# Kernel optimization log

Measured on AMD Instinct MI355X. Metric: run time of the kernel, lower is better.

The kernel has to match this reference:

```python
import jax, jax.numpy as jnp
import numpy as np
from jax import lax

BN_EPS = 1e-5
ARC_EPS = 1e-7
M = 0.5   # margin
S = 64.0  # scale


def _conv_block(x, w, g, b, a, stride):
    # Conv2d(bias=False, VALID) + BatchNorm2d (training mode, batch stats) + PReLU
    y = lax.conv_general_dilated(x, w, (stride, stride), 'VALID',
                                 dimension_numbers=('NCHW', 'OIHW', 'NCHW'))
    mu = y.mean((0, 2, 3), keepdims=True)
    var = ((y - mu) ** 2).mean((0, 2, 3), keepdims=True)
    y = (y - mu) * lax.rsqrt(var + BN_EPS) * g.reshape(1, -1, 1, 1) + b.reshape(1, -1, 1, 1)
    return jnp.where(y > 0, y, a * y)


def setup_inputs() -> dict:
    key = jax.random.key(0)
    ks = jax.random.split(key, 16)
    N = 4096
    d = {}
    d['x'] = jax.random.normal(ks[0], (N, 1, 28, 28), jnp.float32)
    d['labels'] = jax.random.randint(ks[1], (N,), 0, 10)
    conv_shapes = [(32, 1, 1, 1), (64, 32, 3, 3), (32, 64, 1, 1),
                   (64, 32, 3, 3), (32, 64, 1, 1), (64, 32, 3, 3)]
    for i, s in enumerate(conv_shapes):
        fan_in = s[1] * s[2] * s[3]
        d[f'cw{i}'] = jax.random.normal(ks[2 + i], s, jnp.float32) / np.sqrt(fan_in)
        d[f'bg{i}'] = jnp.ones((s[0],), jnp.float32)
        d[f'bb{i}'] = jnp.zeros((s[0],), jnp.float32)
        d[f'pa{i}'] = jnp.full((), 0.25, jnp.float32)  # nn.PReLU() single param
    d['lw1'] = jax.random.normal(ks[8], (128, 1024), jnp.float32) * (1.0 / np.sqrt(1024))
    d['lg1'] = jnp.ones((128,), jnp.float32)
    d['lb1'] = jnp.zeros((128,), jnp.float32)
    d['pl1'] = jnp.full((), 0.25, jnp.float32)
    d['lw2'] = jax.random.normal(ks[9], (2, 128), jnp.float32) * (1.0 / np.sqrt(128))
    d['lb2'] = jnp.zeros((2,), jnp.float32)
    d['aw'] = jax.random.normal(ks[10], (10, 2), jnp.float32) * 0.2  # ArcLoss fc weight (out, in)
    return d


def reference(x, labels, cw0, cw1, cw2, cw3, cw4, cw5,
              bg0, bb0, bg1, bb1, bg2, bb2, bg3, bb3, bg4, bb4, bg5, bb5,
              pa0, pa1, pa2, pa3, pa4, pa5,
              lw1, lg1, lb1, pl1, lw2, lb2, aw):
    strides = (1, 2, 1, 2, 1, 1)
    ws = (cw0, cw1, cw2, cw3, cw4, cw5)
    gs = (bg0, bg1, bg2, bg3, bg4, bg5)
    bs = (bb0, bb1, bb2, bb3, bb4, bb5)
    pas = (pa0, pa1, pa2, pa3, pa4, pa5)
    h = x
    for w, g, b, a, st in zip(ws, gs, bs, pas, strides):
        h = _conv_block(h, w, g, b, a, st)  # final: (N, 64, 4, 4)
    flat = h.reshape(h.shape[0], -1)        # (N, 1024)
    z = flat @ lw1.T                         # (N, 128)
    mu = z.mean(0)
    var = ((z - mu) ** 2).mean(0)
    z = (z - mu) * lax.rsqrt(var + BN_EPS) * lg1 + lb1
    z = jnp.where(z > 0, z, pl1 * z)
    features = z @ lw2.T + lb2               # (N, 2)

    # ArcLoss. NOTE: original torch code's weight-normalization loop is a no-op
    # (rebinds local var), so fc weight is used UN-normalized; only x is normalized.
    xn = features / jnp.linalg.norm(features, axis=-1, keepdims=True)
    wf = xn @ aw.T                           # (N, 10) logits
    n = wf.shape[0]
    tgt = wf[jnp.arange(n), labels]          # vectorized diag gather
    num = S * jnp.cos(jnp.arccos(jnp.clip(tgt, -1.0 + ARC_EPS, 1.0 - ARC_EPS)) + M)
    # vectorized exclusion sum: sum_j exp(s*wf[i,j]) minus the target column
    den = jnp.exp(num) + jnp.sum(jnp.exp(S * wf), axis=1) - jnp.exp(S * tgt)
    loss = -jnp.mean(num - jnp.log(den))
    return (features, wf, loss)
```

## Files before the change

### kernel.cpp

```cpp
#include <hip/hip_runtime.h>
#include <hip/hip_bf16.h>
#include <hip/hip_fp16.h>
#include <math.h>


typedef __attribute__((ext_vector_type(8))) short s16x8;
typedef __attribute__((ext_vector_type(8))) _Float16 f16x8;
typedef __attribute__((ext_vector_type(2))) _Float16 h16x2;
typedef __attribute__((ext_vector_type(16))) float f32x16;

__device__ __forceinline__ unsigned short f2bf(float f) {
  __hip_bfloat16 h = __float2bfloat16(f);
  unsigned short u;
  __builtin_memcpy(&u, &h, 2);
  return u;
}
__device__ __forceinline__ float bf2f(unsigned short h) {
  union { unsigned int u; float f; } t; t.u = ((unsigned int)h) << 16; return t.f;
}
__device__ __forceinline__ unsigned short f2h(float f) {
  _Float16 h = (_Float16)f;
  unsigned short u;
  __builtin_memcpy(&u, &h, 2);
  return u;
}

__device__ void dRedX(const float* __restrict__ x, float* __restrict__ part, int b) {
  int tid = threadIdx.x;
  const float4* x4 = (const float4*)x;
  float s = 0.f, q = 0.f;
  for (size_t i = (size_t)b * 256 + tid; i < 802816; i += (size_t)512 * 256) {
    float4 v = x4[i];
    s += v.x + v.y + v.z + v.w;
    q += v.x * v.x + v.y * v.y + v.z * v.z + v.w * v.w;
  }
#pragma unroll
  for (int off = 32; off; off >>= 1) {
    s += __shfl_down(s, off);
    q += __shfl_down(q, off);
  }
  __shared__ float ls[4][2];
  int w = tid >> 6;
  if ((tid & 63) == 0) { ls[w][0] = s; ls[w][1] = q; }
  __syncthreads();
  if (tid == 0) {
    part[b * 2]     = ls[0][0] + ls[1][0] + ls[2][0] + ls[3][0];
    part[b * 2 + 1] = ls[0][1] + ls[1][1] + ls[2][1] + ls[3][1];
  }
}

__device__ void dPrepW(const float* __restrict__ cw1, unsigned short* __restrict__ wf) {
  int tid = threadIdx.x;
  int lane = tid & 63, fb = tid >> 6;
  int m = lane & 31, kg = lane >> 5;
  for (int pass = 0; pass < 9; pass++) {
    int f = pass * 4 + fb;
    int tap = f >> 2, rem = f & 3, kt = rem >> 1, nt = rem & 1;
    int o = nt * 32 + m;
    int kb = kt * 16 + kg * 8;
    union { s16x8 v; unsigned short e[8]; } u;
#pragma unroll
    for (int j = 0; j < 8; j++)
      u.e[j] = f2h(cw1[(size_t)o * 288 + (size_t)(kb + j) * 9 + tap]);
    ((s16x8*)wf)[f * 64 + lane] = u.v;
  }
}

__device__ void dPrepW3(const float* __restrict__ cw, unsigned short* __restrict__ wf3) {
  int tid = threadIdx.x;
  int lane = tid & 63, fq = tid >> 6;
  int m = lane & 31, kg = lane >> 5;
  for (int pass = 0; pass < 9; pass++) {
    int f = pass * 4 + fq;
    int s = f >> 1, nt = f & 1;
    int tap = s >> 1;
    int o = nt * 32 + m;
    int c0 = (s & 1) * 16 + kg * 8;
    union { s16x8 v; unsigned short e[8]; } u;
#pragma unroll
    for (int j = 0; j < 8; j++)
      u.e[j] = f2h(cw[(size_t)o * 288 + (size_t)(c0 + j) * 9 + tap]);
    ((s16x8*)wf3)[f * 64 + lane] = u.v;
  }
}

__device__ void dPrepW1x1(const float* __restrict__ wgt, unsigned short* __restrict__ wfb) {
  int tid = threadIdx.x;
  int l = tid & 63, ks = tid >> 6;
  int o = l & 31, kg = l >> 5;
  union { s16x8 v; unsigned short e[8]; } u;
#pragma unroll
  for (int j = 0; j < 8; j++) {
    int c = ks * 16 + kg * 8 + j;
    u.e[j] = f2h(wgt[o * 64 + c]);
  }
  ((s16x8*)wfb)[ks * 64 + l] = u.v;
}

__device__ void dPrepLW(const float* __restrict__ lw1, unsigned short* __restrict__ wfl, int blk) {
  int tid = threadIdx.x;
  int lane = tid & 63, fq = tid >> 6;
  int m = lane & 31, kg = lane >> 5;
  for (int pp = 0; pp < 4; pp++) {
    int f_idx = (blk * 4 + pp) * 4 + fq;
    int ks = f_idx >> 2, nt = f_idx & 3;
    int f = nt * 32 + m;
    int kb = ks * 16 + kg * 8;
    const float4* src = (const float4*)(lw1 + (size_t)f * 1024 + kb);
    float4 v0 = src[0], v1 = src[1];
    float t[8] = {v0.x, v0.y, v0.z, v0.w, v1.x, v1.y, v1.z, v1.w};
    union { s16x8 v; unsigned short e[8]; } u;
#pragma unroll
    for (int j = 0; j < 8; j++) u.e[j] = f2bf(t[j]);
    ((s16x8*)wfl)[f_idx * 64 + lane] = u.v;
  }
}

__global__ __launch_bounds__(256) void kSetup(
    const float* __restrict__ x, float* __restrict__ PX,
    const float* __restrict__ cw1, unsigned short* __restrict__ WF,
    const float* __restrict__ cw3, unsigned short* __restrict__ WF3,
    const float* __restrict__ cw5, unsigned short* __restrict__ WF5,
    const float* __restrict__ cw2, unsigned short* __restrict__ WC2,
    const float* __restrict__ cw4, unsigned short* __restrict__ WC4,
    const float* __restrict__ lw1, unsigned short* __restrict__ WFL) {
  int b = blockIdx.x;
  if (b < 512)       dRedX(x, PX, b);
  else if (b == 512) dPrepW(cw1, WF);
  else if (b == 513) dPrepW3(cw3, WF3);
  else if (b == 514) dPrepW3(cw5, WF5);
  else if (b == 515) dPrepW1x1(cw2, WC2);
  else if (b == 516) dPrepW1x1(cw4, WC4);
  else               dPrepLW(lw1, WFL, b - 517);
}

__global__ __launch_bounds__(256) void kRedPart(const float* __restrict__ part,
                                                float* __restrict__ outp, int nb, int C2) {
  int slot = blockIdx.x;
  int tid = threadIdx.x;
  float s = 0.f;
  for (int i = tid; i < nb; i += 256) s += part[(size_t)i * C2 + slot];
#pragma unroll
  for (int off = 32; off; off >>= 1) s += __shfl_down(s, off);
  __shared__ float ls[4];
  if ((tid & 63) == 0) ls[tid >> 6] = s;
  __syncthreads();
  if (tid == 0) outp[slot] = ls[0] + ls[1] + ls[2] + ls[3];
}

__global__ __launch_bounds__(256, 2) void kConv1(
    const float* __restrict__ x, const float* __restrict__ cw0,
    const float* __restrict__ bg0, const float* __restrict__ bb0,
    const float* __restrict__ pa0, const unsigned short* __restrict__ wf,
    const float* __restrict__ sx, unsigned short* __restrict__ y1b,
    float* __restrict__ part) {
  __shared__ __align__(16) unsigned short h0t[13440];
  __shared__ __align__(16) float xbuf[420];
  __shared__ float s0[32], t0[32];
  int tid = threadIdx.x;
  int n = blockIdx.x >> 1, half = blockIdx.x & 1;
  int l = tid & 63, w = tid >> 6;
  int nt = w & 1, mpair = w >> 1;
  int m = l & 31, kg = l >> 5;
  int npos = half ? 78 : 91;
  int xoff = half ? 392 : 0;
  int nxpix = half ? 364 : 420;

  f16x8 bfr[9][2];
  const f16x8* wfp = (const f16x8*)wf;
#pragma unroll
  for (int tap = 0; tap < 9; tap++)
#pragma unroll
    for (int kt = 0; kt < 2; kt++)
      bfr[tap][kt] = wfp[(tap * 4 + kt * 2 + nt) * 64 + l];

  {
    int nx4 = half ? 91 : 105;
    if (tid < nx4)
      ((float4*)xbuf)[tid] = ((const float4*)(x + (size_t)n * 784 + xoff))[tid];
  }
  if (tid < 32) {
    const float invM = 1.0f / (4096.0f * 784.0f);
    float mux = sx[0] * invM;
    float varx = fmaxf(sx[1] * invM - mux * mux, 0.0f);
    float w0 = cw0[tid];
    float inv = rsqrtf(w0 * w0 * varx + 1e-5f);
    float sc = w0 * bg0[tid] * inv;
    s0[tid] = sc;
    t0[tid] = bb0[tid] - mux * sc;
  }
  __syncthreads();

  float a0p = *pa0;
  _Float16 a1h = (_Float16)a0p;
  h16x2 a2 = {a1h, a1h};
  h16x2 z2 = {(_Float16)0.0f, (_Float16)0.0f};
  int g = tid & 3;
  h16x2 sg2[4], tg2[4];
#pragma unroll
  for (int j = 0; j < 4; j++) {
    sg2[j] = (h16x2){(_Float16)s0[g * 8 + 2 * j], (_Float16)s0[g * 8 + 2 * j + 1]};
    tg2[j] = (h16x2){(_Float16)t0[g * 8 + 2 * j], (_Float16)t0[g * 8 + 2 * j + 1]};
  }
  char* h0b = (char*)h0t;
  int koffW = g * 16;
  for (int t = 0; t < 7; t++) {
    int p = (tid >> 2) + t * 64;
    if (p < nxpix) {
      _Float16 xh = (_Float16)xbuf[p];
      h16x2 x2 = {xh, xh};
      union { f16x8 v; h16x2 h2[4]; } u;
#pragma unroll
      for (int j = 0; j < 4; j++) {
        h16x2 tv = x2 * sg2[j] + tg2[j];
        u.h2[j] = a2 * __builtin_elementwise_min(tv, z2) +
                  __builtin_elementwise_max(tv, z2);
      }
      int ad = ((p << 6) + koffW) ^ (((p >> 1) & 7) << 4);
      *(f16x8*)(h0b + ad) = u.v;
    }
  }
  __syncthreads();

  int tA = mpair ? 2 : 0;
  int lpA = tA * 32 + m; lpA = lpA > npos - 1 ? npos - 1 : lpA;
  int lpB = 32 + m;      lpB = lpB > npos - 1 ? npos - 1 : lpB;
  int pixbA = (lpA / 13) * 56 + (lpA % 13) * 2;
  int pixbB = (lpB / 13) * 56 + (lpB % 13) * 2;
  int koffA = kg * 16;

#define Z16 {0.f,0.f,0.f,0.f, 0.f,0.f,0.f,0.f, 0.f,0.f,0.f,0.f, 0.f,0.f,0.f,0.f}
  f32x16 acc0 = Z16, acc1 = Z16;

#define MT_STEP(ACC, PB) { \
  _Pragma("unroll") for (int tap = 0; tap < 9; tap++) { \
    int pix = (PB) + (tap / 3) * 28 + (tap % 3); \
    int ad = ((pix << 6) + koffA) ^ (((pix >> 1) & 7) << 4); \
    f16x8 a0 = *(const f16x8*)(h0b + ad); \
    f16x8 a1 = *(const f16x8*)(h0b + (ad ^ 32)); \
    ACC = __builtin_amdgcn_mfma_f32_32x32x16_f16(a0, bfr[tap][0], ACC, 0, 0, 0); \
    ACC = __builtin_amdgcn_mfma_f32_32x32x16_f16(a1, bfr[tap][1], ACC, 0, 0, 0); \
  } }

  MT_STEP(acc0, pixbA)
  if (mpair == 0) { MT_STEP(acc1, pixbB) }
#undef MT_STEP

  __syncthreads();
  unsigned short* ystage = h0t;
  float* sSf = xbuf;
  float* sQf = xbuf + 128;
  float s = 0.f, q = 0.f;
  int och = nt * 32 + m;
#define ST_MT(ACC, TILE) { int pbase = (TILE) * 32 + (kg << 2); \
  _Pragma("unroll") for (int r = 0; r < 16; r++) { \
    int p = pbase + (r & 3) + ((r >> 2) << 3); \
    if (p < npos) { float v = ACC[r]; \
      ystage[p * 64 + och] = f2h(v); s += v; q += v * v; } } }

  ST_MT(acc0, tA)
  if (mpair == 0) { ST_MT(acc1, 1) }
#undef ST_MT

  s += __shfl_xor(s, 32);
  q += __shfl_xor(q, 32);
  if (l < 32) { sSf[w * 32 + l] = s; sQf[w * 32 + l] = q; }
  __syncthreads();
  {
    int nseg = npos * 8;
    const s16x8* src8 = (const s16x8*)ystage;
    s16x8* dst8 = (s16x8*)(y1b + (size_t)n * 10816 + half * 5824);
    for (int e = tid; e < nseg; e += 256) dst8[e] = src8[e];
  }
  if (tid < 64) {
    int o = tid, wv = o >> 5;
    part[(size_t)blockIdx.x * 128 + o] =
        sSf[wv * 32 + (o & 31)] + sSf[(wv + 2) * 32 + (o & 31)];
  } else if (tid < 128) {
    int o = tid - 64, wv = o >> 5;
    part[(size_t)blockIdx.x * 128 + 64 + o] =
        sQf[wv * 32 + (o & 31)] + sQf[(wv + 2) * 32 + (o & 31)];
  }
}

__global__ __launch_bounds__(256, 4) void kConv1x1m(
    const unsigned short* __restrict__ wfb, const float* __restrict__ g,
    const float* __restrict__ b, const float* __restrict__ pa,
    const float* __restrict__ stats, float invM,
    const unsigned short* __restrict__ in, unsigned short* __restrict__ outb,
    float* __restrict__ part) {
  __shared__ __align__(16) unsigned short hs[128 * 64];
  __shared__ float scs[64], shs[64];
  __shared__ float sS[4][32], sQ[4][32];
  int tid = threadIdx.x;
  size_t r0 = (size_t)blockIdx.x * 128;
  int l = tid & 63, w = tid >> 6;
  int m = l & 31, kg = l >> 5;

  f16x8 bfr[4];
  const f16x8* bp = (const f16x8*)wfb;
#pragma unroll
  for (int ks = 0; ks < 4; ks++) bfr[ks] = bp[ks * 64 + l];

  if (tid < 64) {
    float mu = stats[tid] * invM;
    float va = fmaxf(stats[64 + tid] * invM - mu * mu, 0.0f);
    float iv = rsqrtf(va + 1e-5f);
    float sc = g[tid] * iv;
    scs[tid] = sc;
    shs[tid] = b[tid] - mu * sc;
  }
  __syncthreads();
  float al = *pa;
  _Float16 alh = (_Float16)al;
  h16x2 a2 = {alh, alh};
  h16x2 z2 = {(_Float16)0.0f, (_Float16)0.0f};
  int seg0 = tid & 7;
  h16x2 sc2[4], sh2[4];
#pragma unroll
  for (int j = 0; j < 4; j++) {
    int c = seg0 * 8 + 2 * j;
    sc2[j] = (h16x2){(_Float16)scs[c], (_Float16)scs[c + 1]};
    sh2[j] = (h16x2){(_Float16)shs[c], (_Float16)shs[c + 1]};
  }
  char* hb = (char*)hs;
#pragma unroll
  for (int i = 0; i < 4; i++) {
    int e = tid + i * 256;
    int row = e >> 3;
    union { f16x8 v; h16x2 h2[4]; } u, o8;
    u.v = *(const f16x8*)(in + (r0 + row) * 64 + seg0 * 8);
#pragma unroll
    for (int j = 0; j < 4; j++) {
      h16x2 tv = u.h2[j] * sc2[j] + sh2[j];
      o8.h2[j] = a2 * __builtin_elementwise_min(tv, z2) +
                 __builtin_elementwise_max(tv, z2);
    }
    int ad = (row * 128 + seg0 * 16) ^ ((row & 7) << 4);
    *(f16x8*)(hb + ad) = o8.v;
  }
  __syncthreads();

#define Z16 {0.f,0.f,0.f,0.f, 0.f,0.f,0.f,0.f, 0.f,0.f,0.f,0.f, 0.f,0.f,0.f,0.f}
  f32x16 acc = Z16;
#undef Z16
  int rloc = w * 32 + m;
  int abase = (rloc * 128 + kg * 16) ^ ((rloc & 7) << 4);
#pragma unroll
  for (int ks = 0; ks < 4; ks++) {
    f16x8 a = *(const f16x8*)(hb + (abase ^ (ks * 32)));
    acc = __builtin_amdgcn_mfma_f32_32x32x16_f16(a, bfr[ks], acc, 0, 0, 0);
  }

  float ss = 0.f, qq = 0.f;
#pragma unroll
  for (int rr = 0; rr < 16; rr++) {
    int rowt = (rr & 3) + ((rr >> 2) << 3) + (kg << 2);
    float v = acc[rr];
    outb[(r0 + (size_t)w * 32 + rowt) * 32 + m] = f2h(v);
    ss += v; qq += v * v;
  }
  ss += __shfl_xor(ss, 32);
  qq += __shfl_xor(qq, 32);
  if (l < 32) { sS[w][l] = ss; sQ[w][l] = qq; }
  __syncthreads();
  if (tid < 32) {
    part[(size_t)blockIdx.x * 64 + tid] = sS[0][tid] + sS[1][tid] + sS[2][tid] + sS[3][tid];
  } else if (tid < 64) {
    int o = tid - 32;
    part[(size_t)blockIdx.x * 64 + 32 + o] = sQ[0][o] + sQ[1][o] + sQ[2][o] + sQ[3][o];
  }
}

__global__ __launch_bounds__(256, 3) void kConv3m(
    const unsigned short* __restrict__ wf3, const float* __restrict__ g,
    const float* __restrict__ b, const float* __restrict__ pa,
    const float* __restrict__ stats, const unsigned short* __restrict__ in,
    unsigned short* __restrict__ outb, float* __restrict__ part) {
  __shared__ __align__(16) unsigned short h2t[169 * 32];
  __shared__ float scs[32], shs[32];
  __shared__ float sS[4][32], sQ[4][32];
  int tid = threadIdx.x;
  int n = blockIdx.x;
  int l = tid & 63, w = tid >> 6;
  int nt = w & 1, mt = w >> 1;
  int m = l & 31, kg = l >> 5;

  f16x8 bfr[18];
  const f16x8* wfp = (const f16x8*)wf3;
#pragma unroll
  for (int s = 0; s < 18; s++) bfr[s] = wfp[(s * 2 + nt) * 64 + l];

  if (tid < 32) {
    const float invM = 1.0f / 692224.0f;
    float mu = stats[tid] * invM;
    float va = fmaxf(stats[32 + tid] * invM - mu * mu, 0.0f);
    float iv = rsqrtf(va + 1e-5f);
    float sc = g[tid] * iv;
    scs[tid] = sc;
    shs[tid] = b[tid] - mu * sc;
  }
  __syncthreads();
  float al = *pa;
  _Float16 alh = (_Float16)al;
  h16x2 a2 = {alh, alh};
  h16x2 z2 = {(_Float16)0.0f, (_Float16)0.0f};
  int q0 = tid & 3;
  h16x2 sc2[4], sh2[4];
#pragma unroll
  for (int j = 0; j < 4; j++) {
    int c = q0 * 8 + 2 * j;
    sc2[j] = (h16x2){(_Float16)scs[c], (_Float16)scs[c + 1]};
    sh2[j] = (h16x2){(_Float16)shs[c], (_Float16)shs[c + 1]};
  }
  char* hb = (char*)h2t;
  for (int e = tid; e < 676; e += 256) {
    int p = e >> 2;
    union { f16x8 v; h16x2 h2[4]; } u, o8;
    u.v = ((const f16x8*)(in + ((size_t)n * 169 + p) * 32))[q0];
#pragma unroll
    for (int j = 0; j < 4; j++) {
      h16x2 tv = u.h2[j] * sc2[j] + sh2[j];
      o8.h2[j] = a2 * __builtin_elementwise_min(tv, z2) +
                 __builtin_elementwise_max(tv, z2);
    }
    int ad = ((p << 6) + q0 * 16) ^ (((p >> 1) & 7) << 4);
    *(f16x8*)(hb + ad) = o8.v;
  }
  __syncthreads();

  int p = mt * 32 + m;
  p = p > 35 ? 35 : p;
  int pixb = (p / 6) * 26 + (p % 6) * 2;

#define Z16 {0.f,0.f,0.f,0.f, 0.f,0.f,0.f,0.f, 0.f,0.f,0.f,0.f, 0.f,0.f,0.f,0.f}
  f32x16 acc = Z16;
#undef Z16
#pragma unroll
  for (int s = 0; s < 18; s++) {
    int tap = s >> 1;
    int pix = pixb + (tap / 3) * 13 + (tap % 3);
    int ad = ((pix << 6) + (s & 1) * 32 + kg * 16) ^ (((pix >> 1) & 7) << 4);
    f16x8 a = *(const f16x8*)(hb + ad);
    acc = __builtin_amdgcn_mfma_f32_32x32x16_f16(a, bfr[s], acc, 0, 0, 0);
  }

  float ss = 0.f, qq = 0.f;
  int och = nt * 32 + m;
#pragma unroll
  for (int r = 0; r < 16; r++) {
    int row = (r & 3) + ((r >> 2) << 3) + (kg << 2);
    int pp = mt * 32 + row;
    if (pp < 36) {
      float v = acc[r];
      outb[((size_t)n * 36 + pp) * 64 + och] = f2h(v);
      ss += v; qq += v * v;
    }
  }
  ss += __shfl_xor(ss, 32);
  qq += __shfl_xor(qq, 32);
  if (l < 32) { sS[w][l] = ss; sQ[w][l] = qq; }
  __syncthreads();
  if (tid < 64) {
    int o = tid, wv = o >> 5;
    part[(size_t)n * 128 + o] = sS[wv][o & 31] + sS[wv + 2][o & 31];
  } else if (tid < 128) {
    int o = tid - 64, wv = o >> 5;
    part[(size_t)n * 128 + 64 + o] = sQ[wv][o & 31] + sQ[wv + 2][o & 31];
  }
}

__global__ __launch_bounds__(128) void kConv5m(
    const unsigned short* __restrict__ wf5, const float* __restrict__ g,
    const float* __restrict__ b, const float* __restrict__ pa,
    const float* __restrict__ stats, const unsigned short* __restrict__ in,
    float* __restrict__ outb, float* __restrict__ part) {
  __shared__ __align__(16) unsigned short h4t[2 * 1280];
  __shared__ float scs[32], shs[32];
  int tid = threadIdx.x;
  int nA = blockIdx.x * 2;
  int l = tid & 63, w = tid >> 6;
  int m = l & 31, kg = l >> 5;

  f16x8 bfr[18];
  const f16x8* wfp = (const f16x8*)wf5;
#pragma unroll
  for (int s = 0; s < 18; s++) bfr[s] = wfp[(s * 2 + w) * 64 + l];

  if (tid < 32) {
    const float invM = 1.0f / 147456.0f;
    float mu = stats[tid] * invM;
    float va = fmaxf(stats[32 + tid] * invM - mu * mu, 0.0f);
    float iv = rsqrtf(va + 1e-5f);
    float sc = g[tid] * iv;
    scs[tid] = sc;
    shs[tid] = b[tid] - mu * sc;
  }
  __syncthreads();
  float al = *pa;
  _Float16 alh = (_Float16)al;
  h16x2 a2 = {alh, alh};
  h16x2 z2 = {(_Float16)0.0f, (_Float16)0.0f};
  int q0 = tid & 3;
  h16x2 sc2[4], sh2[4];
#pragma unroll
  for (int j = 0; j < 4; j++) {
    int c = q0 * 8 + 2 * j;
    sc2[j] = (h16x2){(_Float16)scs[c], (_Float16)scs[c + 1]};
    sh2[j] = (h16x2){(_Float16)shs[c], (_Float16)shs[c + 1]};
  }
  char* hb = (char*)h4t;
  for (int e = tid; e < 288; e += 128) {
    int img = e >= 144;
    int rem = e - img * 144;
    int p = rem >> 2;
    union { f16x8 v; h16x2 h2[4]; } u, o8;
    u.v = ((const f16x8*)(in + ((size_t)(nA + img) * 36 + p) * 32))[q0];
#pragma unroll
    for (int j = 0; j < 4; j++) {
      h16x2 tv = u.h2[j] * sc2[j] + sh2[j];
      o8.h2[j] = a2 * __builtin_elementwise_min(tv, z2) +
                 __builtin_elementwise_max(tv, z2);
    }
    int ad = img * 2560 + (((p << 6) + q0 * 16) ^ (((p >> 1) & 7) << 4));
    *(f16x8*)(hb + ad) = o8.v;
  }
  __syncthreads();

  int imgl = m >> 4;
  int pl = m & 15;
  int pixb = (pl >> 2) * 6 + (pl & 3);
  int ibase = imgl * 2560;

#define Z16 {0.f,0.f,0.f,0.f, 0.f,0.f,0.f,0.f, 0.f,0.f,0.f,0.f, 0.f,0.f,0.f,0.f}
  f32x16 acc = Z16;
#undef Z16
#pragma unroll
  for (int s = 0; s < 18; s++) {
    int tap = s >> 1;
    int pix = pixb + (tap / 3) * 6 + (tap % 3);
    int ad = ibase + (((pix << 6) + (s & 1) * 32 + kg * 16) ^ (((pix >> 1) & 7) << 4));
    f16x8 a = *(const f16x8*)(hb + ad);
    acc = __builtin_amdgcn_mfma_f32_32x32x16_f16(a, bfr[s], acc, 0, 0, 0);
  }

  float ss = 0.f, qq = 0.f;
  int och = w * 32 + m;
#pragma unroll
  for (int r = 0; r < 16; r++) {
    int row = (r & 3) + ((r >> 2) << 3) + (kg << 2);
    int img = row >> 4, p = row & 15;
    float v = acc[r];
    outb[(size_t)(nA + img) * 1024 + och * 16 + p] = v;
    ss += v; qq += v * v;
  }
  ss += __shfl_xor(ss, 32);
  qq += __shfl_xor(qq, 32);
  if (l < 32) {
    part[(size_t)blockIdx.x * 128 + w * 32 + l] = ss;
    part[(size_t)blockIdx.x * 128 + 64 + w * 32 + l] = qq;
  }
}

__global__ __launch_bounds__(128) void kFC1m(
    const unsigned short* __restrict__ wfl, const float* __restrict__ g,
    const float* __restrict__ b, const float* __restrict__ pa,
    const float* __restrict__ stats, const float* __restrict__ y5,
    float* __restrict__ z, float* __restrict__ part) {
  __shared__ __align__(16) unsigned short hs[32 * 1024];
  __shared__ float scs[64], shs[64];
  int tid = threadIdx.x;
  int n0 = blockIdx.x * 32;
  if (tid < 64) {
    const float invM = 1.0f / 65536.0f;
    float mu = stats[tid] * invM;
    float va = fmaxf(stats[64 + tid] * invM - mu * mu, 0.0f);
    float iv = rsqrtf(va + 1e-5f);
    float sc = g[tid] * iv;
    scs[tid] = sc;
    shs[tid] = b[tid] - mu * sc;
  }
  __syncthreads();
  float al = *pa;
  char* hb = (char*)hs;
  for (int i = 0; i < 32; i++) {
    int sgi = tid + i * 128;
    int nn = sgi >> 7, k8 = sgi & 127;
    int c = k8 >> 1;
    float sc = scs[c], sh = shs[c];
    const float4* src = (const float4*)(y5 + (size_t)(n0 + nn) * 1024 + k8 * 8);
    float4 v0 = src[0], v1 = src[1];
    float t[8] = {v0.x, v0.y, v0.z, v0.w, v1.x, v1.y, v1.z, v1.w};
    union { s16x8 v; unsigned short e[8]; } u;
#pragma unroll
    for (int j = 0; j < 8; j++) {
      float h = fmaf(t[j], sc, sh);
      h = h > 0.f ? h : al * h;
      u.e[j] = f2bf(h);
    }
    int ad = (nn * 2048 + k8 * 16) ^ ((nn & 7) << 4);
    *(s16x8*)(hb + ad) = u.v;
  }
  __syncthreads();

  int l = tid & 63, w = tid >> 6;
  int m = l & 31, kg = l >> 5;
#define Z16 {0.f,0.f,0.f,0.f, 0.f,0.f,0.f,0.f, 0.f,0.f,0.f,0.f, 0.f,0.f,0.f,0.f}
  f32x16 acc0 = Z16, acc1 = Z16;
#undef Z16
  const s16x8* bp = (const s16x8*)wfl;
  int abase = (m * 2048 + kg * 16) ^ ((m & 7) << 4);
#pragma unroll 4
  for (int ks = 0; ks < 64; ks++) {
    s16x8 a = *(const s16x8*)(hb + (abase ^ (ks * 32)));
    s16x8 b0 = bp[(ks * 4 + 2 * w + 0) * 64 + l];
    s16x8 b1 = bp[(ks * 4 + 2 * w + 1) * 64 + l];
    acc0 = __builtin_amdgcn_mfma_f32_32x32x16_bf16(a, b0, acc0, 0, 0, 0);
    acc1 = __builtin_amdgcn_mfma_f32_32x32x16_bf16(a, b1, acc1, 0, 0, 0);
  }

  float s0 = 0.f, q0 = 0.f, s1 = 0.f, q1 = 0.f;
  int f0c = (2 * w) * 32 + m, f1c = (2 * w + 1) * 32 + m;
#pragma unroll
  for (int r = 0; r < 16; r++) {
    int n = (r & 3) + ((r >> 2) << 3) + (kg << 2);
    float v0 = acc0[r], v1 = acc1[r];
    z[(size_t)(n0 + n) * 128 + f0c] = v0;
    z[(size_t)(n0 + n) * 128 + f1c] = v1;
    s0 += v0; q0 += v0 * v0; s1 += v1; q1 += v1 * v1;
  }
  s0 += __shfl_xor(s0, 32); q0 += __shfl_xor(q0, 32);
  s1 += __shfl_xor(s1, 32); q1 += __shfl_xor(q1, 32);
  if (l < 32) {
    size_t base = (size_t)blockIdx.x * 256;
    part[base + w * 64 + m] = s0;
    part[base + w * 64 + 32 + m] = s1;
    part[base + 128 + w * 64 + m] = q0;
    part[base + 128 + w * 64 + 32 + m] = q1;
  }
}

__global__ __launch_bounds__(256) void kFC2Arc(
    const float* __restrict__ z, const float* __restrict__ s6,
    const float* __restrict__ lg1, const float* __restrict__ lb1,
    const float* __restrict__ pl1, const float* __restrict__ lw2,
    const float* __restrict__ lb2, const float* __restrict__ aw,
    const int* __restrict__ labels, float* __restrict__ out,
    float* __restrict__ lpart) {
  __shared__ float scz[128], shz[128], w2a[128], w2b[128];
  __shared__ float awl[20];
  __shared__ float lred[4];
  int tid = threadIdx.x;
  if (tid < 128) {
    const float invM = 1.0f / 4096.0f;
    float mu = s6[tid] * invM;
    float va = fmaxf(s6[128 + tid] * invM - mu * mu, 0.0f);
    float iv = rsqrtf(va + 1e-5f);
    float sc = lg1[tid] * iv;
    scz[tid] = sc;
    shz[tid] = lb1[tid] - mu * sc;
    w2a[tid] = lw2[tid];
    w2b[tid] = lw2[128 + tid];
  }
  if (tid < 20) awl[tid] = aw[tid];
  __syncthreads();
  float al = *pl1;
  int n = blockIdx.x * 256 + tid;
  const float4* zr = (const float4*)(z + (size_t)n * 128);
  float f0 = lb2[0], f1 = lb2[1];
#pragma unroll
  for (int kb = 0; kb < 32; kb++) {
    float4 v = zr[kb];
    float hv[4] = {v.x, v.y, v.z, v.w};
#pragma unroll
    for (int u = 0; u < 4; u++) {
      int k = kb * 4 + u;
      float h = fmaf(hv[u], scz[k], shz[k]);
      h = h > 0.f ? h : al * h;
      f0 = fmaf(h, w2a[k], f0);
      f1 = fmaf(h, w2b[k], f1);
    }
  }
  out[(size_t)n * 2] = f0;
  out[(size_t)n * 2 + 1] = f1;
  float nrm = sqrtf(fmaxf(f0 * f0 + f1 * f1, 1e-30f));
  float xn0 = f0 / nrm, xn1 = f1 / nrm;
  int lab = labels[n];
  float wv[10];
  float m64 = -3.4e38f;
#pragma unroll
  for (int j = 0; j < 10; j++) {
    float w = xn0 * awl[2 * j] + xn1 * awl[2 * j + 1];
    wv[j] = w;
    out[8192 + (size_t)n * 10 + j] = w;
    m64 = fmaxf(m64, 64.0f * w);
  }
  float tgt = wv[0];
#pragma unroll
  for (int j = 1; j < 10; j++) if (j == lab) tgt = wv[j];
  if (lab == 0) tgt = wv[0];
  const float CLO = (float)(-1.0 + 1e-7);
  const float CHI = (float)(1.0 - 1e-7);
  float t = fminf(fmaxf(tgt, CLO), CHI);
  float num = 64.0f * (t * 0.87758256189037276f - 0.47942553860420301f * sqrtf(fmaxf(1.0f - t * t, 0.0f)));
  float L = fmaxf(num, m64);
  float dsum = expf(num - L) - expf(64.0f * tgt - L);
#pragma unroll
  for (int j = 0; j < 10; j++) dsum += expf(64.0f * wv[j] - L);
  dsum = fmaxf(dsum, 1e-30f);
  float li = num - (L + logf(dsum));
#pragma unroll
  for (int off = 32; off; off >>= 1) li += __shfl_down(li, off);
  if ((tid & 63) == 0) lred[tid >> 6] = li;
  __syncthreads();
  if (tid == 0) lpart[blockIdx.x] = lred[0] + lred[1] + lred[2] + lred[3];
}

__global__ void kFinal(const float* __restrict__ lpart, float* __restrict__ out) {
  int tid = threadIdx.x;
  float v = (tid < 16) ? lpart[tid] : 0.f;
#pragma unroll
  for (int off = 8; off; off >>= 1) v += __shfl_down(v, off);
  if (tid == 0) out[49152] = -v * (1.0f / 4096.0f);
}

extern "C" void kernel_launch(void* const* d_in, const int* in_sizes, int n_in,
                              void* d_out, int out_size, void* d_ws, size_t ws_size,
                              hipStream_t stream) {
  const float* x   = (const float*)d_in[0];
  const int* labels = (const int*)d_in[1];
  const float* cw0 = (const float*)d_in[2];
  const float* bg0 = (const float*)d_in[3];
  const float* bb0 = (const float*)d_in[4];
  const float* pa0 = (const float*)d_in[5];
  const float* cw1 = (const float*)d_in[6];
  const float* bg1 = (const float*)d_in[7];
  const float* bb1 = (const float*)d_in[8];
  const float* pa1 = (const float*)d_in[9];
  const float* cw2 = (const float*)d_in[10];
  const float* bg2 = (const float*)d_in[11];
  const float* bb2 = (const float*)d_in[12];
  const float* pa2 = (const float*)d_in[13];
  const float* cw3 = (const float*)d_in[14];
  const float* bg3 = (const float*)d_in[15];
  const float* bb3 = (const float*)d_in[16];
  const float* pa3 = (const float*)d_in[17];
  const float* cw4 = (const float*)d_in[18];
  const float* bg4 = (const float*)d_in[19];
  const float* bb4 = (const float*)d_in[20];
  const float* pa4 = (const float*)d_in[21];
  const float* cw5 = (const float*)d_in[22];
  const float* bg5 = (const float*)d_in[23];
  const float* bb5 = (const float*)d_in[24];
  const float* pa5 = (const float*)d_in[25];
  const float* lw1 = (const float*)d_in[26];
  const float* lg1 = (const float*)d_in[27];
  const float* lb1 = (const float*)d_in[28];
  const float* pl1 = (const float*)d_in[29];
  const float* lw2 = (const float*)d_in[30];
  const float* lb2 = (const float*)d_in[31];
  const float* aw  = (const float*)d_in[32];
  float* out = (float*)d_out;
  float* ws = (float*)d_ws;

  float* PX = ws;
  float* SX = ws + 1024;
  float* S1 = ws + 1040;
  float* S2 = ws + 1168;
  float* S3 = ws + 1232;
  float* S4 = ws + 1360;
  float* S5 = ws + 1424;
  float* S6 = ws + 1552;
  float* LP = ws + 1808;
  float* P1 = ws + 2048;
  float* P2 = P1 + 1048576;
  float* P3 = P2 + 346112;
  float* P4 = P3 + 524288;
  float* P5 = P4 + 73728;
  float* P6 = P1;
  unsigned short* Y1 = (unsigned short*)(ws + (size_t)2359296);
  unsigned short* Y2 = Y1 + (size_t)44302336;
  unsigned short* Y3 = Y2 + (size_t)22151168;
  unsigned short* Y4 = Y3 + (size_t)9437184;
  float* Y5 = (float*)(Y4 + (size_t)4718592);
  float* Z  = Y5 + (size_t)4194304;
  float* WF = Z + 524288;
  float* WFL = WF + 16384;
  float* WF3 = WFL + 65536;
  float* WC2 = WF3 + 16384;
  float* WC4 = WC2 + 1024;
  float* WF5 = WC4 + 1024;

  kSetup<<<533, 256, 0, stream>>>(x, PX, cw1, (unsigned short*)WF,
                                  cw3, (unsigned short*)WF3,
                                  cw5, (unsigned short*)WF5,
                                  cw2, (unsigned short*)WC2,
                                  cw4, (unsigned short*)WC4,
                                  lw1, (unsigned short*)WFL);
  kRedPart<<<2, 256, 0, stream>>>(PX, SX, 512, 2);
  kConv1<<<8192, 256, 0, stream>>>(x, cw0, bg0, bb0, pa0, (const unsigned short*)WF, SX, Y1, P1);
  kRedPart<<<128, 256, 0, stream>>>(P1, S1, 8192, 128);
  kConv1x1m<<<5408, 256, 0, stream>>>((const unsigned short*)WC2, bg1, bb1, pa1, S1,
                                      1.0f / 692224.0f, Y1, Y2, P2);
  kRedPart<<<64, 256, 0, stream>>>(P2, S2, 5408, 64);
  kConv3m<<<4096, 256, 0, stream>>>((const unsigned short*)WF3, bg2, bb2, pa2, S2, Y2, Y3, P3);
  kRedPart<<<128, 256, 0, stream>>>(P3, S3, 4096, 128);
  kConv1x1m<<<1152, 256, 0, stream>>>((const unsigned short*)WC4, bg3, bb3, pa3, S3,
                                      1.0f / 147456.0f, Y3, Y4, P4);
  kRedPart<<<64, 256, 0, stream>>>(P4, S4, 1152, 64);
  kConv5m<<<2048, 128, 0, stream>>>((const unsigned short*)WF5, bg4, bb4, pa4, S4, Y4, Y5, P5);
  kRedPart<<<128, 256, 0, stream>>>(P5, S5, 2048, 128);
  kFC1m<<<128, 128, 0, stream>>>((const unsigned short*)WFL, bg5, bb5, pa5, S5, Y5, Z, P6);
  kRedPart<<<256, 256, 0, stream>>>(P6, S6, 128, 256);
  kFC2Arc<<<16, 256, 0, stream>>>(Z, S6, lg1, lb1, pl1, lw2, lb2, aw, labels, out, LP);
  kFinal<<<1, 64, 0, stream>>>(LP, out);
}
```

Measured before the change: 209.1 us.

## Fuse input-stat reduction into conv1, drop LDS staging, store Y5 as fp16

The separate two-slot reduction kernel is removed, and each conv1 block now reduces the 512 partial input sums itself, which costs one launch but repeats a small reduction in every block. The 1x1 conv kernel no longer stages BN+PReLU-transformed activations in shared memory. Each lane loads its own A fragment from global memory and applies the affine and PReLU in registers right before the MFMA, removing an LDS round trip and a barrier. The conv5 output is stored as fp16 instead of fp32, halving that tensor's traffic, and FC1 now uses fp16 weights and an fp16 MFMA. FC1 also splits output features across twice as many blocks with in-register activation transforms, which adds more redundant A loads and lowers precision.

```diff
diff --git a/kernel.cpp b/kernel.cpp
--- a/kernel.cpp
+++ b/kernel.cpp
@@ -111,7 +111,7 @@
     float t[8] = {v0.x, v0.y, v0.z, v0.w, v1.x, v1.y, v1.z, v1.w};
     union { s16x8 v; unsigned short e[8]; } u;
 #pragma unroll
-    for (int j = 0; j < 8; j++) u.e[j] = f2bf(t[j]);
+    for (int j = 0; j < 8; j++) u.e[j] = f2h(t[j]);
     ((s16x8*)wfl)[f_idx * 64 + lane] = u.v;
   }
 }
@@ -152,11 +152,12 @@
     const float* __restrict__ x, const float* __restrict__ cw0,
     const float* __restrict__ bg0, const float* __restrict__ bb0,
     const float* __restrict__ pa0, const unsigned short* __restrict__ wf,
-    const float* __restrict__ sx, unsigned short* __restrict__ y1b,
+    const float* __restrict__ PX, unsigned short* __restrict__ y1b,
     float* __restrict__ part) {
   __shared__ __align__(16) unsigned short h0t[13440];
   __shared__ __align__(16) float xbuf[420];
   __shared__ float s0[32], t0[32];
+  __shared__ float sxr[8];
   int tid = threadIdx.x;
   int n = blockIdx.x >> 1, half = blockIdx.x & 1;
   int l = tid & 63, w = tid >> 6;
@@ -179,10 +180,23 @@
     if (tid < nx4)
       ((float4*)xbuf)[tid] = ((const float4*)(x + (size_t)n * 784 + xoff))[tid];
   }
+  {
+    float rs = PX[tid * 2]     + PX[(tid + 256) * 2];
+    float rq = PX[tid * 2 + 1] + PX[(tid + 256) * 2 + 1];
+#pragma unroll
+    for (int off = 32; off; off >>= 1) {
+      rs += __shfl_down(rs, off);
+      rq += __shfl_down(rq, off);
+    }
+    if ((tid & 63) == 0) { sxr[(tid >> 6) * 2] = rs; sxr[(tid >> 6) * 2 + 1] = rq; }
+  }
+  __syncthreads();
   if (tid < 32) {
+    float sxs = sxr[0] + sxr[2] + sxr[4] + sxr[6];
+    float sxq = sxr[1] + sxr[3] + sxr[5] + sxr[7];
     const float invM = 1.0f / (4096.0f * 784.0f);
-    float mux = sx[0] * invM;
-    float varx = fmaxf(sx[1] * invM - mux * mux, 0.0f);
+    float mux = sxs * invM;
+    float varx = fmaxf(sxq * invM - mux * mux, 0.0f);
     float w0 = cw0[tid];
     float inv = rsqrtf(w0 * w0 * varx + 1e-5f);
     float sc = w0 * bg0[tid] * inv;
@@ -289,7 +303,6 @@
     const float* __restrict__ stats, float invM,
     const unsigned short* __restrict__ in, unsigned short* __restrict__ outb,
     float* __restrict__ part) {
-  __shared__ __align__(16) unsigned short hs[128 * 64];
   __shared__ float scs[64], shs[64];
   __shared__ float sS[4][32], sQ[4][32];
   int tid = threadIdx.x;
@@ -315,41 +328,33 @@
   _Float16 alh = (_Float16)al;
   h16x2 a2 = {alh, alh};
   h16x2 z2 = {(_Float16)0.0f, (_Float16)0.0f};
-  int seg0 = tid & 7;
-  h16x2 sc2[4], sh2[4];
-#pragma unroll
-  for (int j = 0; j < 4; j++) {
-    int c = seg0 * 8 + 2 * j;
-    sc2[j] = (h16x2){(_Float16)scs[c], (_Float16)scs[c + 1]};
-    sh2[j] = (h16x2){(_Float16)shs[c], (_Float16)shs[c + 1]};
-  }
-  char* hb = (char*)hs;
-#pragma unroll
-  for (int i = 0; i < 4; i++) {
-    int e = tid + i * 256;
-    int row = e >> 3;
-    union { f16x8 v; h16x2 h2[4]; } u, o8;
-    u.v = *(const f16x8*)(in + (r0 + row) * 64 + seg0 * 8);
+  h16x2 sc2[4][4], sh2[4][4];
+#pragma unroll
+  for (int ks = 0; ks < 4; ks++)
 #pragma unroll
     for (int j = 0; j < 4; j++) {
-      h16x2 tv = u.h2[j] * sc2[j] + sh2[j];
-      o8.h2[j] = a2 * __builtin_elementwise_min(tv, z2) +
-                 __builtin_elementwise_max(tv, z2);
+      int c = ks * 16 + kg * 8 + 2 * j;
+      sc2[ks][j] = (h16x2){(_Float16)scs[c], (_Float16)scs[c + 1]};
+      sh2[ks][j] = (h16x2){(_Float16)shs[c], (_Float16)shs[c + 1]};
     }
-    int ad = (row * 128 + seg0 * 16) ^ ((row & 7) << 4);
-    *(f16x8*)(hb + ad) = o8.v;
-  }
-  __syncthreads();
+
+  int rloc = w * 32 + m;
+  const f16x8* arow = (const f16x8*)(in + (r0 + rloc) * 64);
 
 #define Z16 {0.f,0.f,0.f,0.f, 0.f,0.f,0.f,0.f, 0.f,0.f,0.f,0.f, 0.f,0.f,0.f,0.f}
   f32x16 acc = Z16;
 #undef Z16
-  int rloc = w * 32 + m;
-  int abase = (rloc * 128 + kg * 16) ^ ((rloc & 7) << 4);
 #pragma unroll
   for (int ks = 0; ks < 4; ks++) {
-    f16x8 a = *(const f16x8*)(hb + (abase ^ (ks * 32)));
-    acc = __builtin_amdgcn_mfma_f32_32x32x16_f16(a, bfr[ks], acc, 0, 0, 0);
+    union { f16x8 v; h16x2 h2[4]; } ui, ua;
+    ui.v = arow[ks * 2 + kg];
+#pragma unroll
+    for (int j = 0; j < 4; j++) {
+      h16x2 tv = ui.h2[j] * sc2[ks][j] + sh2[ks][j];
+      ua.h2[j] = a2 * __builtin_elementwise_min(tv, z2) +
+                 __builtin_elementwise_max(tv, z2);
+    }
+    acc = __builtin_amdgcn_mfma_f32_32x32x16_f16(ua.v, bfr[ks], acc, 0, 0, 0);
   }
 
   float ss = 0.f, qq = 0.f;
@@ -474,7 +479,7 @@
     const unsigned short* __restrict__ wf5, const float* __restrict__ g,
     const float* __restrict__ b, const float* __restrict__ pa,
     const float* __restrict__ stats, const unsigned short* __restrict__ in,
-    float* __restrict__ outb, float* __restrict__ part) {
+    unsigned short* __restrict__ outb, float* __restrict__ part) {
   __shared__ __align__(16) unsigned short h4t[2 * 1280];
   __shared__ float scs[32], shs[32];
   int tid = threadIdx.x;
@@ -551,7 +556,7 @@
     int row = (r & 3) + ((r >> 2) << 3) + (kg << 2);
     int img = row >> 4, p = row & 15;
     float v = acc[r];
-    outb[(size_t)(nA + img) * 1024 + och * 16 + p] = v;
+    outb[(size_t)(nA + img) * 1024 + och * 16 + p] = f2h(v);
     ss += v; qq += v * v;
   }
   ss += __shfl_xor(ss, 32);
@@ -565,12 +570,14 @@
 __global__ __launch_bounds__(128) void kFC1m(
     const unsigned short* __restrict__ wfl, const float* __restrict__ g,
     const float* __restrict__ b, const float* __restrict__ pa,
-    const float* __restrict__ stats, const float* __restrict__ y5,
+    const float* __restrict__ stats, const unsigned short* __restrict__ y5,
     float* __restrict__ z, float* __restrict__ part) {
-  __shared__ __align__(16) unsigned short hs[32 * 1024];
   __shared__ float scs[64], shs[64];
   int tid = threadIdx.x;
-  int n0 = blockIdx.x * 32;
+  int nb = blockIdx.x >> 1, fh = blockIdx.x & 1;
+  int n0 = nb * 32;
+  int l = tid & 63, w = tid >> 6;
+  int m = l & 31, kg = l >> 5;
   if (tid < 64) {
     const float invM = 1.0f / 65536.0f;
     float mu = stats[tid] * invM;
@@ -582,61 +589,49 @@
   }
   __syncthreads();
   float al = *pa;
-  char* hb = (char*)hs;
-  for (int i = 0; i < 32; i++) {
-    int sgi = tid + i * 128;
-    int nn = sgi >> 7, k8 = sgi & 127;
-    int c = k8 >> 1;
-    float sc = scs[c], sh = shs[c];
-    const float4* src = (const float4*)(y5 + (size_t)(n0 + nn) * 1024 + k8 * 8);
-    float4 v0 = src[0], v1 = src[1];
-    float t[8] = {v0.x, v0.y, v0.z, v0.w, v1.x, v1.y, v1.z, v1.w};
-    union { s16x8 v; unsigned short e[8]; } u;
-#pragma unroll
-    for (int j = 0; j < 8; j++) {
-      float h = fmaf(t[j], sc, sh);
-      h = h > 0.f ? h : al * h;
-      u.e[j] = f2bf(h);
-    }
-    int ad = (nn * 2048 + k8 * 16) ^ ((nn & 7) << 4);
-    *(s16x8*)(hb + ad) = u.v;
-  }
-  __syncthreads();
-
-  int l = tid & 63, w = tid >> 6;
-  int m = l & 31, kg = l >> 5;
+  _Float16 alh = (_Float16)al;
+  h16x2 a2 = {alh, alh};
+  h16x2 z2 = {(_Float16)0.0f, (_Float16)0.0f};
+  int t = fh * 2 + w;
+  const f16x8* bp = (const f16x8*)wfl;
+  const f16x8* arow = (const f16x8*)(y5 + (size_t)(n0 + m) * 1024);
+
 #define Z16 {0.f,0.f,0.f,0.f, 0.f,0.f,0.f,0.f, 0.f,0.f,0.f,0.f, 0.f,0.f,0.f,0.f}
-  f32x16 acc0 = Z16, acc1 = Z16;
+  f32x16 acc = Z16;
 #undef Z16
-  const s16x8* bp = (const s16x8*)wfl;
-  int abase = (m * 2048 + kg * 16) ^ ((m & 7) << 4);
 #pragma unroll 4
   for (int ks = 0; ks < 64; ks++) {
-    s16x8 a = *(const s16x8*)(hb + (abase ^ (ks * 32)));
-    s16x8 b0 = bp[(ks * 4 + 2 * w + 0) * 64 + l];
-    s16x8 b1 = bp[(ks * 4 + 2 * w + 1) * 64 + l];
-    acc0 = __builtin_amdgcn_mfma_f32_32x32x16_bf16(a, b0, acc0, 0, 0, 0);
-    acc1 = __builtin_amdgcn_mfma_f32_32x32x16_bf16(a, b1, acc1, 0, 0, 0);
-  }
-
-  float s0 = 0.f, q0 = 0.f, s1 = 0.f, q1 = 0.f;
-  int f0c = (2 * w) * 32 + m, f1c = (2 * w + 1) * 32 + m;
+    _Float16 sch = (_Float16)scs[ks];
+    _Float16 shh = (_Float16)shs[ks];
+    h16x2 sc2 = {sch, sch};
+    h16x2 sh2 = {shh, shh};
+    union { f16x8 v; h16x2 h2[4]; } ui, ua;
+    ui.v = arow[ks * 2 + kg];
+#pragma unroll
+    for (int j = 0; j < 4; j++) {
+      h16x2 tv = ui.h2[j] * sc2 + sh2;
+      ua.h2[j] = a2 * __builtin_elementwise_min(tv, z2) +
+                 __builtin_elementwise_max(tv, z2);
+    }
+    f16x8 bv = bp[(ks * 4 + t) * 64 + l];
+    acc = __builtin_amdgcn_mfma_f32_32x32x16_f16(ua.v, bv, acc, 0, 0, 0);
+  }
+
+  float s0 = 0.f, q0 = 0.f;
+  int f = fh * 64 + w * 32 + m;
 #pragma unroll
   for (int r = 0; r < 16; r++) {
     int n = (r & 3) + ((r >> 2) << 3) + (kg << 2);
-    float v0 = acc0[r], v1 = acc1[r];
-    z[(size_t)(n0 + n) * 128 + f0c] = v0;
-    z[(size_t)(n0 + n) * 128 + f1c] = v1;
-    s0 += v0; q0 += v0 * v0; s1 += v1; q1 += v1 * v1;
-  }
-  s0 += __shfl_xor(s0, 32); q0 += __shfl_xor(q0, 32);
-  s1 += __shfl_xor(s1, 32); q1 += __shfl_xor(q1, 32);
+    float v = acc[r];
+    z[(size_t)(n0 + n) * 128 + f] = v;
+    s0 += v; q0 += v * v;
+  }
+  s0 += __shfl_xor(s0, 32);
+  q0 += __shfl_xor(q0, 32);
   if (l < 32) {
-    size_t base = (size_t)blockIdx.x * 256;
-    part[base + w * 64 + m] = s0;
-    part[base + w * 64 + 32 + m] = s1;
-    part[base + 128 + w * 64 + m] = q0;
-    part[base + 128 + w * 64 + 32 + m] = q1;
+    size_t base = (size_t)nb * 256;
+    part[base + fh * 64 + w * 32 + l] = s0;
+    part[base + 128 + fh * 64 + w * 32 + l] = q0;
   }
 }
 
@@ -764,7 +759,6 @@
   float* ws = (float*)d_ws;
 
   float* PX = ws;
-  float* SX = ws + 1024;
   float* S1 = ws + 1040;
   float* S2 = ws + 1168;
   float* S3 = ws + 1232;
@@ -782,8 +776,8 @@
   unsigned short* Y2 = Y1 + (size_t)44302336;
   unsigned short* Y3 = Y2 + (size_t)22151168;
   unsigned short* Y4 = Y3 + (size_t)9437184;
-  float* Y5 = (float*)(Y4 + (size_t)4718592);
-  float* Z  = Y5 + (size_t)4194304;
+  unsigned short* Y5 = Y4 + (size_t)4718592;
+  float* Z  = (float*)(Y5 + (size_t)4194304);
   float* WF = Z + 524288;
   float* WFL = WF + 16384;
   float* WF3 = WFL + 65536;
@@ -797,8 +791,8 @@
                                   cw2, (unsigned short*)WC2,
                                   cw4, (unsigned short*)WC4,
                                   lw1, (unsigned short*)WFL);
-  kRedPart<<<2, 256, 0, stream>>>(PX, SX, 512, 2);
-  kConv1<<<8192, 256, 0, stream>>>(x, cw0, bg0, bb0, pa0, (const unsigned short*)WF, SX, Y1, P1);
+  kConv1<<<8192, 256, 0, stream>>>(x, cw0, bg0, bb0, pa0, (const unsigned short*)WF,
+                                   PX, Y1, P1);
   kRedPart<<<128, 256, 0, stream>>>(P1, S1, 8192, 128);
   kConv1x1m<<<5408, 256, 0, stream>>>((const unsigned short*)WC2, bg1, bb1, pa1, S1,
                                       1.0f / 692224.0f, Y1, Y2, P2);
@@ -810,7 +804,7 @@
   kRedPart<<<64, 256, 0, stream>>>(P4, S4, 1152, 64);
   kConv5m<<<2048, 128, 0, stream>>>((const unsigned short*)WF5, bg4, bb4, pa4, S4, Y4, Y5, P5);
   kRedPart<<<128, 256, 0, stream>>>(P5, S5, 2048, 128);
-  kFC1m<<<128, 128, 0, stream>>>((const unsigned short*)WFL, bg5, bb5, pa5, S5, Y5, Z, P6);
+  kFC1m<<<256, 128, 0, stream>>>((const unsigned short*)WFL, bg5, bb5, pa5, S5, Y5, Z, P6);
   kRedPart<<<256, 256, 0, stream>>>(P6, S6, 128, 256);
   kFC2Arc<<<16, 256, 0, stream>>>(Z, S6, lg1, lb1, pl1, lw2, lb2, aw, labels, out, LP);
   kFinal<<<1, 64, 0, stream>>>(LP, out);
```

Result: faster. 202.4 us (-3.2%).
